# Kernel optimization log

Measured on AMD Instinct MI355X. Metric: run time of the kernel, lower is better.

The kernel has to match this reference:

```python
import jax, jax.numpy as jnp
import numpy as np

EPS = 1e-5
NUM_HEADS = 12
MAX_TEXT_LEN = 40

def ln(x, g, b):
    m = x.mean(-1, keepdims=True)
    v = ((x - m) ** 2).mean(-1, keepdims=True)
    return (x - m) / jnp.sqrt(v + EPS) * g + b

def mlp(x, w1, b1, w2, b2):
    h = jax.nn.gelu(x @ w1.T + b1, approximate=False)  # torch nn.GELU default = exact
    return h @ w2.T + b2

def setup_inputs() -> dict:
    key = jax.random.key(0)
    ks = jax.random.split(key, 16)
    B, N, C, H, HID = 16, 616, 768, 12, 3072
    s = 0.02
    d = {}
    d["x"] = jax.random.normal(ks[0], (B, N, C), jnp.float32)
    d["rel_bias"] = jax.random.normal(ks[1], (H, N, N), jnp.float32)
    d["ln1_g"] = jnp.ones(C, jnp.float32); d["ln1_b"] = jnp.zeros(C, jnp.float32)
    d["w_qkv"] = jax.random.normal(ks[2], (3 * C, C), jnp.float32) * s
    d["q_bias"] = jnp.zeros(C, jnp.float32); d["v_bias"] = jnp.zeros(C, jnp.float32)
    d["w_proj"] = jax.random.normal(ks[3], (C, C), jnp.float32) * s
    d["b_proj"] = jnp.zeros(C, jnp.float32)
    d["gamma1"] = 0.1 * jnp.ones(C, jnp.float32)
    d["gamma2"] = 0.1 * jnp.ones(C, jnp.float32)
    d["ln2t_g"] = jnp.ones(C, jnp.float32); d["ln2t_b"] = jnp.zeros(C, jnp.float32)
    d["ln2i_g"] = jnp.ones(C, jnp.float32); d["ln2i_b"] = jnp.zeros(C, jnp.float32)
    d["wt1"] = jax.random.normal(ks[4], (HID, C), jnp.float32) * s
    d["bt1"] = jnp.zeros(HID, jnp.float32)
    d["wt2"] = jax.random.normal(ks[5], (C, HID), jnp.float32) * s
    d["bt2"] = jnp.zeros(C, jnp.float32)
    d["wi1"] = jax.random.normal(ks[6], (HID, C), jnp.float32) * s
    d["bi1"] = jnp.zeros(HID, jnp.float32)
    d["wi2"] = jax.random.normal(ks[7], (C, HID), jnp.float32) * s
    d["bi2"] = jnp.zeros(C, jnp.float32)
    return d

def reference(x, rel_bias, ln1_g, ln1_b, w_qkv, q_bias, v_bias, w_proj, b_proj,
              gamma1, gamma2, ln2t_g, ln2t_b, ln2i_g, ln2i_b,
              wt1, bt1, wt2, bt2, wi1, bi1, wi2, bi2):
    B, N, C = x.shape
    H = NUM_HEADS
    hd = C // H
    scale = hd ** -0.5
    # --- attention ---
    n = ln(x, ln1_g, ln1_b)
    qkv_bias = jnp.concatenate([q_bias, jnp.zeros_like(v_bias), v_bias])
    qkv = (n @ w_qkv.T + qkv_bias).reshape(B, N, 3, H, hd).transpose(2, 0, 3, 1, 4)
    q, k, v = qkv[0] * scale, qkv[1], qkv[2]  # [B,H,N,hd]
    attn = jnp.einsum('bhqd,bhkd->bhqk', q.astype(jnp.float32), k.astype(jnp.float32))
    attn = attn + rel_bias  # rel_bias [H,N,N] broadcasts over B
    attn = jax.nn.softmax(attn, axis=-1).astype(x.dtype)
    o = jnp.einsum('bhqk,bhkd->bhqd', attn, v).transpose(0, 2, 1, 3).reshape(B, N, C)
    o = o @ w_proj.T + b_proj
    x = x + gamma1 * o
    # --- modality-split MLP (modality_type is None, no vl-ffn) ---
    xt = x[:, :MAX_TEXT_LEN]
    xi = x[:, MAX_TEXT_LEN:]
    xt = xt + gamma2 * mlp(ln(xt, ln2t_g, ln2t_b), wt1, bt1, wt2, bt2)
    xi = xi + gamma2 * mlp(ln(xi, ln2i_g, ln2i_b), wi1, bi1, wi2, bi2)
    return jnp.concatenate([xt, xi], axis=1)
```

## Files before the change

### kernel.cpp

```cpp
#include <hip/hip_runtime.h>
#include <hip/hip_bf16.h>
#include <stdint.h>
#include <math.h>

#define AS1 __attribute__((address_space(1)))
#define AS3 __attribute__((address_space(3)))

typedef __bf16 bf16_t;
typedef __bf16 bf16x8 __attribute__((ext_vector_type(8)));
typedef float f32x4 __attribute__((ext_vector_type(4)));

static constexpr int B_ = 16, N_ = 616, C_ = 768, H_ = 12, HD = 64, HID = 3072;
static constexpr int NP = 640;
static constexpr int M_REAL = B_ * N_;
static constexpr int M_PAD = 9984;
static constexpr int NT_ = 40, NI_ = 576;

__device__ __forceinline__ void gl_lds16(const void* g, void* l) {
  __builtin_amdgcn_global_load_lds((const AS1 void*)(uintptr_t)g,
                                   (AS3 void*)(uint32_t)(uintptr_t)l, 16, 0, 0);
}
__device__ __forceinline__ f32x4 mfma16(bf16x8 a, bf16x8 b, f32x4 c) {
  return __builtin_amdgcn_mfma_f32_16x16x32_bf16(a, b, c, 0, 0, 0);
}
__device__ __forceinline__ float gelu_f(float x) {
  float u = x * (0.7978845608f + 0.0356774081f * x * x);
  return x / (1.f + __expf(-2.f * u));
}

struct CastArgs {
  const float* src[7];
  bf16_t* dst[7];
  int n4[7];
};

__global__ __launch_bounds__(256) void cast_all(CastArgs a, int total4) {
  int i = blockIdx.x * blockDim.x + threadIdx.x;
  int st = gridDim.x * blockDim.x;
  for (; i < total4; i += st) {
    int off = i;
#pragma unroll
    for (int s = 0; s < 7; ++s) {
      if (off < a.n4[s]) {
        float4 v = ((const float4*)a.src[s])[off];
        float sub = (s == 6) ? 8.f : 0.f;
        bf16_t* d = a.dst[s] + (size_t)off * 4;
        d[0] = (bf16_t)(v.x - sub); d[1] = (bf16_t)(v.y - sub);
        d[2] = (bf16_t)(v.z - sub); d[3] = (bf16_t)(v.w - sub);
        break;
      }
      off -= a.n4[s];
    }
  }
}

__global__ __launch_bounds__(256) void ln_rows(const float* __restrict__ x,
                                               const float* __restrict__ g,
                                               const float* __restrict__ b,
                                               bf16_t* __restrict__ out) {
  int r = blockIdx.x, t = threadIdx.x;
  bf16_t* orow = out + (size_t)r * C_;
  const float* xr = x + (size_t)r * C_;
  float v0 = xr[t], v1 = xr[t + 256], v2 = xr[t + 512];
  float s = v0 + v1 + v2, ss = v0 * v0 + v1 * v1 + v2 * v2;
#pragma unroll
  for (int off = 32; off > 0; off >>= 1) { s += __shfl_xor(s, off); ss += __shfl_xor(ss, off); }
  __shared__ float sm[8];
  int w = t >> 6;
  if ((t & 63) == 0) { sm[w] = s; sm[4 + w] = ss; }
  __syncthreads();
  s = sm[0] + sm[1] + sm[2] + sm[3];
  ss = sm[4] + sm[5] + sm[6] + sm[7];
  float mean = s * (1.f / C_);
  float var = ss * (1.f / C_) - mean * mean;
  float ri = rsqrtf(var + 1e-5f);
  orow[t]       = (bf16_t)((v0 - mean) * ri * g[t]       + b[t]);
  orow[t + 256] = (bf16_t)((v1 - mean) * ri * g[t + 256] + b[t + 256]);
  orow[t + 512] = (bf16_t)((v2 - mean) * ri * g[t + 512] + b[t + 512]);
}

__global__ __launch_bounds__(256) void ln2_pack(const float* __restrict__ x1,
                                                const float* __restrict__ gt, const float* __restrict__ bt,
                                                const float* __restrict__ gi, const float* __restrict__ bi,
                                                bf16_t* __restrict__ out) {
  int m = blockIdx.x, t = threadIdx.x;
  if (m >= M_REAL) {
    bf16_t* orow = out + (size_t)(640 + (m - M_REAL)) * C_;
    orow[t] = (bf16_t)0.f; orow[t+256] = (bf16_t)0.f; orow[t+512] = (bf16_t)0.f;
    return;
  }
  int b_ = m / N_, nn = m - b_ * N_;
  const float* g; const float* bb; int dest;
  if (nn < NT_) { dest = b_ * NT_ + nn; g = gt; bb = bt; }
  else          { dest = 768 + b_ * NI_ + (nn - NT_); g = gi; bb = bi; }
  const float* xr = x1 + (size_t)m * C_;
  float v0 = xr[t], v1 = xr[t + 256], v2 = xr[t + 512];
  float s = v0 + v1 + v2, ss = v0 * v0 + v1 * v1 + v2 * v2;
#pragma unroll
  for (int off = 32; off > 0; off >>= 1) { s += __shfl_xor(s, off); ss += __shfl_xor(ss, off); }
  __shared__ float sm[8];
  int w = t >> 6;
  if ((t & 63) == 0) { sm[w] = s; sm[4 + w] = ss; }
  __syncthreads();
  s = sm[0] + sm[1] + sm[2] + sm[3];
  ss = sm[4] + sm[5] + sm[6] + sm[7];
  float mean = s * (1.f / C_);
  float var = ss * (1.f / C_) - mean * mean;
  float ri = rsqrtf(var + 1e-5f);
  bf16_t* orow = out + (size_t)dest * C_;
  orow[t]       = (bf16_t)((v0 - mean) * ri * g[t]       + bb[t]);
  orow[t + 256] = (bf16_t)((v1 - mean) * ri * g[t + 256] + bb[t + 256]);
  orow[t + 512] = (bf16_t)((v2 - mean) * ri * g[t + 512] + bb[t + 512]);
}

__global__ __launch_bounds__(256) void transpose_v(const bf16_t* __restrict__ v,
                                                   bf16_t* __restrict__ vT) {
  __shared__ bf16_t t[64][80];
  int n0 = blockIdx.x * 64, bh = blockIdx.y;
  int tid = threadIdx.x;
  int r0 = tid >> 2, c0 = (tid & 3) * 16;
  int n = n0 + r0;
#pragma unroll
  for (int cc = 0; cc < 2; ++cc) {
    bf16x8 vv;
    if (n < N_) vv = *(const bf16x8*)(v + ((size_t)bh * N_ + n) * HD + c0 + cc * 8);
    else {
#pragma unroll
      for (int e = 0; e < 8; ++e) vv[e] = (bf16_t)0.f;
    }
#pragma unroll
    for (int e = 0; e < 8; ++e) t[c0 + cc * 8 + e][r0] = vv[e];
  }
  __syncthreads();
  int d = tid >> 2, nc = (tid & 3) * 16;
  bf16_t* dst = vT + ((size_t)(bh * HD + d)) * NP + n0 + nc;
  *(bf16x8*)dst       = *(const bf16x8*)&t[d][nc];
  *(bf16x8*)(dst + 8) = *(const bf16x8*)&t[d][nc + 8];
}

struct EpiP {
  const float* bias;
  const float* bias_i;
  const float* bias2;
  const float* gamma;
  const float* xres;
  float* outf;
  bf16_t* ob0;
  bf16_t* ob1;
  bf16_t* ob2;
};

template <int EPI>
__global__ __launch_bounds__(256, 3) void gemm128(const bf16_t* __restrict__ A,
                                                  const bf16_t* __restrict__ Bt,
                                                  const bf16_t* __restrict__ Bi,
                                                  int K, int MBc, int nb, int tb, EpiP P) {
  __shared__ bf16_t As[8192], Bs[8192];
  const int tid = threadIdx.x, lane = tid & 63, w = tid >> 6;
  const int l16 = lane & 15, lq = lane >> 4;
  const int wr = w >> 1, wc = w & 1;
  const int NTk = K >> 6;

  int mblk, nblk;
  {
    int nwg = MBc * nb;
    int bid = blockIdx.x;
    int q8 = nwg >> 3, r8 = nwg & 7;
    int xcd = bid & 7, sidx = bid >> 3;
    int wg = (xcd < r8 ? xcd * (q8 + 1) : r8 * (q8 + 1) + (xcd - r8) * q8) + sidx;
    mblk = wg / nb; nblk = wg - mblk * nb;
  }
  const int m0 = mblk * 128, n0 = nblk * 128;
  const bf16_t* Bw = (mblk < tb) ? Bt : Bi;

  f32x4 acc[4][4] = {};

  const int swsrc = ((lane & 7) ^ ((lane >> 3) & 7)) * 8;
  size_t aoff[4], boff[4];
  int ldsoff[4];
#pragma unroll
  for (int j = 0; j < 4; ++j) {
    int srow = j * 32 + w * 8 + (lane >> 3);
    aoff[j] = (size_t)(m0 + srow) * K + swsrc;
    boff[j] = (size_t)(n0 + srow) * K + swsrc;
    ldsoff[j] = (j * 256 + w * 64) * 8;
  }
  const int sw0 = ((0 * 4 + lq) ^ (l16 & 7)) * 8;
  const int sw1 = ((1 * 4 + lq) ^ (l16 & 7)) * 8;
  const int rbA = (wr * 64 + l16) * 64;
  const int rbB = (wc * 64 + l16) * 64;

  for (int t = 0; t < NTk; ++t) {
    const size_t kadd = (size_t)t * 64;
#pragma unroll
    for (int j = 0; j < 4; ++j) gl_lds16(A + aoff[j] + kadd, As + ldsoff[j]);
#pragma unroll
    for (int j = 0; j < 4; ++j) gl_lds16(Bw + boff[j] + kadd, Bs + ldsoff[j]);
    __syncthreads();

    bf16x8 av[4][2], bv[4][2];
#pragma unroll
    for (int i = 0; i < 4; ++i) {
      av[i][0] = *(const bf16x8*)(As + rbA + i * 1024 + sw0);
      av[i][1] = *(const bf16x8*)(As + rbA + i * 1024 + sw1);
      bv[i][0] = *(const bf16x8*)(Bs + rbB + i * 1024 + sw0);
      bv[i][1] = *(const bf16x8*)(Bs + rbB + i * 1024 + sw1);
    }
#pragma unroll
    for (int kk = 0; kk < 2; ++kk)
#pragma unroll
      for (int i = 0; i < 4; ++i)
#pragma unroll
        for (int j = 0; j < 4; ++j)
          acc[i][j] = mfma16(av[i][kk], bv[j][kk], acc[i][j]);
    __syncthreads();
  }

  const float* bsel = (mblk < tb) ? P.bias : P.bias_i;
  (void)bsel;
  int which = n0 / C_;
#pragma unroll
  for (int i = 0; i < 4; ++i) {
    int mb = m0 + wr * 64 + i * 16 + lq * 4;
#pragma unroll
    for (int j = 0; j < 4; ++j) {
      int jc = n0 + wc * 64 + j * 16 + l16;
#pragma unroll
      for (int rr = 0; rr < 4; ++rr) {
        int m = mb + rr;
        float v = acc[i][j][rr];
        if constexpr (EPI == 0) {
          int b_ = m / N_, nn = m - b_ * N_;
          int jj = jc - which * C_;
          int hh = jj >> 6, d = jj & 63;
          int bh = b_ * H_ + hh;
          if (which == 0) {
            P.ob0[((size_t)bh * NP + nn) * HD + d] = (bf16_t)((v + P.bias[jj]) * 0.125f);
          } else if (which == 1) {
            P.ob1[((size_t)bh * NP + nn) * HD + d] = (bf16_t)v;
          } else {
            P.ob2[((size_t)bh * N_ + nn) * HD + d] = (bf16_t)(v + P.bias2[jj]);
          }
        } else if constexpr (EPI == 1) {
          size_t idx = (size_t)m * C_ + jc;
          P.outf[idx] = P.xres[idx] + P.gamma[jc] * (v + P.bias[jc]);
        } else if constexpr (EPI == 2) {
          P.ob0[(size_t)m * HID + jc] = (bf16_t)gelu_f(v + bsel[jc]);
        } else {
          int orig = -1;
          if (m < 640)      orig = (m / NT_) * N_ + (m - (m / NT_) * NT_);
          else if (m >= 768) {
            int mi = m - 768;
            int bb = mi / NI_;
            orig = bb * N_ + NT_ + (mi - bb * NI_);
          }
          if (orig >= 0) {
            size_t idx = (size_t)orig * C_ + jc;
            P.outf[idx] = P.xres[idx] + P.gamma[jc] * (v + bsel[jc]);
          }
        }
      }
    }
  }
}

__global__ __launch_bounds__(256) void attn_fwd(const bf16_t* __restrict__ qb,
                                                const bf16_t* __restrict__ kb,
                                                const bf16_t* __restrict__ vT,
                                                const bf16_t* __restrict__ biasb,
                                                bf16_t* __restrict__ o_mat) {
  __shared__ bf16_t qs[64 * 64];
  __shared__ bf16_t ks[2][64 * 64], vs[2][64 * 64];
  __shared__ bf16_t ps[4][16 * 72];
  const int tid = threadIdx.x, lane = tid & 63, w = tid >> 6;
  const int l16 = lane & 15, lq = lane >> 4;
  int wg = (blockIdx.x & 7) * 240 + (blockIdx.x >> 3);
  const int qt = wg % 10;
  const int rb = wg / 10;
  const int b_ = rb & 15, h = rb >> 4;
  const int bh = b_ * H_ + h;
  const int q0 = qt * 64;
  const int swr = (l16 & 7);
  constexpr int NKT = NP / 64;

  const bf16_t* ksrc = kb + (size_t)bh * NP * HD;
  const bf16_t* vsrc = vT + (size_t)bh * HD * NP;

  auto stage_kv = [&](int c, int kt) {
    int n0k = kt * 64;
#pragma unroll
    for (int it = 0; it < 2; ++it) {
      int cb = it * 256 + w * 64, cc = cb + lane;
      int row = cc >> 3, sg = (cc & 7) ^ ((cc >> 3) & 7);
      gl_lds16(ksrc + ((size_t)(n0k + row)) * HD + sg * 8, ks[c] + cb * 8);
      gl_lds16(vsrc + (size_t)row * NP + n0k + sg * 8, vs[c] + cb * 8);
    }
  };

  const bf16_t* qsrc = qb + ((size_t)bh * NP + q0) * HD;
#pragma unroll
  for (int it = 0; it < 2; ++it) {
    int cb = it * 256 + w * 64, c = cb + lane;
    int row = c >> 3, sg = (c & 7) ^ ((c >> 3) & 7);
    gl_lds16(qsrc + row * 64 + sg * 8, qs + cb * 8);
  }
  stage_kv(0, 0);
  __syncthreads();

  bf16x8 aq[2];
  aq[0] = *(const bf16x8*)(qs + (w * 16 + l16) * 64 + ((0 * 4 + lq) ^ swr) * 8);
  aq[1] = *(const bf16x8*)(qs + (w * 16 + l16) * 64 + ((1 * 4 + lq) ^ swr) * 8);

  float lsum[4] = {0.f, 0.f, 0.f, 0.f};
  f32x4 oacc[4] = {};
  const int qrow_base = q0 + w * 16 + lq * 4;

  const bf16_t* bp[4];
#pragma unroll
  for (int r = 0; r < 4; ++r) {
    int qg = qrow_base + r;
    int qc = qg < N_ ? qg : (N_ - 1);
    bp[r] = biasb + (size_t)h * N_ * N_ + (size_t)qc * N_;
  }

  for (int kt = 0; kt < NKT; ++kt) {
    const int c = kt & 1;
    if (kt > 0) __syncthreads();
    if (kt + 1 < NKT) stage_kv(c ^ 1, kt + 1);

    f32x4 sf[4];
#pragma unroll
    for (int f = 0; f < 4; ++f) {
      f32x4 z = {};
#pragma unroll
      for (int kk = 0; kk < 2; ++kk) {
        bf16x8 bk = *(const bf16x8*)(ks[c] + (f * 16 + l16) * 64 + ((kk * 4 + lq) ^ swr) * 8);
        z = mfma16(aq[kk], bk, z);
      }
      sf[f] = z;
    }

    int n0k = kt * 64;
    bf16_t* psw = ps[w];
    if (kt < NKT - 1) {
#pragma unroll
      for (int f = 0; f < 4; ++f) {
        int kc = n0k + f * 16 + l16;
#pragma unroll
        for (int r = 0; r < 4; ++r) {
          float p = __expf(sf[f][r] + (float)bp[r][kc]);
          lsum[r] += p;
          psw[(lq * 4 + r) * 72 + f * 16 + l16] = (bf16_t)p;
        }
      }
    } else {
#pragma unroll
      for (int f = 0; f < 4; ++f) {
        int kc = n0k + f * 16 + l16;
        bool ok = kc < N_;
        int kcs = ok ? kc : 0;
#pragma unroll
        for (int r = 0; r < 4; ++r) {
          float p = ok ? __expf(sf[f][r] + (float)bp[r][kcs]) : 0.f;
          lsum[r] += p;
          psw[(lq * 4 + r) * 72 + f * 16 + l16] = (bf16_t)p;
        }
      }
    }

#pragma unroll
    for (int kk = 0; kk < 2; ++kk) {
      bf16x8 pa = *(const bf16x8*)(psw + l16 * 72 + kk * 32 + lq * 8);
#pragma unroll
      for (int df = 0; df < 4; ++df) {
        bf16x8 bv = *(const bf16x8*)(vs[c] + (df * 16 + l16) * 64 + ((kk * 4 + lq) ^ swr) * 8);
        oacc[df] = mfma16(pa, bv, oacc[df]);
      }
    }
  }

#pragma unroll
  for (int off = 1; off < 16; off <<= 1)
#pragma unroll
    for (int r = 0; r < 4; ++r)
      lsum[r] += __shfl_xor(lsum[r], off, 16);

#pragma unroll
  for (int r = 0; r < 4; ++r) {
    int qg = qrow_base + r;
    if (qg < N_) {
      float rl = 1.f / lsum[r];
      size_t orow = ((size_t)(b_ * N_ + qg)) * C_ + h * HD;
#pragma unroll
      for (int df = 0; df < 4; ++df)
        o_mat[orow + df * 16 + l16] = (bf16_t)(oacc[df][r] * rl);
    }
  }
}

extern "C" void kernel_launch(void* const* d_in, const int* in_sizes, int n_in,
                              void* d_out, int out_size, void* d_ws, size_t ws_size,
                              hipStream_t stream) {
  const float* x      = (const float*)d_in[0];
  const float* rel    = (const float*)d_in[1];
  const float* ln1_g  = (const float*)d_in[2];
  const float* ln1_b  = (const float*)d_in[3];
  const float* w_qkv  = (const float*)d_in[4];
  const float* q_bias = (const float*)d_in[5];
  const float* v_bias = (const float*)d_in[6];
  const float* w_proj = (const float*)d_in[7];
  const float* b_proj = (const float*)d_in[8];
  const float* gamma1 = (const float*)d_in[9];
  const float* gamma2 = (const float*)d_in[10];
  const float* ln2t_g = (const float*)d_in[11];
  const float* ln2t_b = (const float*)d_in[12];
  const float* ln2i_g = (const float*)d_in[13];
  const float* ln2i_b = (const float*)d_in[14];
  const float* wt1    = (const float*)d_in[15];
  const float* bt1    = (const float*)d_in[16];
  const float* wt2    = (const float*)d_in[17];
  const float* bt2    = (const float*)d_in[18];
  const float* wi1    = (const float*)d_in[19];
  const float* bi1    = (const float*)d_in[20];
  const float* wi2    = (const float*)d_in[21];
  const float* bi2    = (const float*)d_in[22];
  float* out = (float*)d_out;

  char* ws = (char*)d_ws;
  bf16_t* wqkvb  = (bf16_t*)(ws + 0);
  bf16_t* wprojb = (bf16_t*)(ws + 3538944);
  bf16_t* wt1b   = (bf16_t*)(ws + 4718592);
  bf16_t* wi1b   = (bf16_t*)(ws + 9437184);
  bf16_t* wt2b   = (bf16_t*)(ws + 14155776);
  bf16_t* wi2b   = (bf16_t*)(ws + 18874368);
  bf16_t* n1     = (bf16_t*)(ws + 23592960);
  float*  x1     = (float*) (ws + 38928384);
  bf16_t* qbuf   = (bf16_t*)(ws + 69206016);
  bf16_t* kbuf   = (bf16_t*)(ws + 84934656);
  bf16_t* vTbuf  = (bf16_t*)(ws + 100663296);
  bf16_t* biasb  = (bf16_t*)(ws + 116391936);
  bf16_t* vtmp   = (bf16_t*)(ws + 38928384);
  bf16_t* o_mat  = n1;
  bf16_t* n2p    = n1;
  bf16_t* hbuf   = qbuf;

  {
    CastArgs a;
    a.src[0] = w_qkv;  a.dst[0] = wqkvb;  a.n4[0] = (3 * C_ * C_) / 4;
    a.src[1] = w_proj; a.dst[1] = wprojb; a.n4[1] = (C_ * C_) / 4;
    a.src[2] = wt1;    a.dst[2] = wt1b;   a.n4[2] = (HID * C_) / 4;
    a.src[3] = wi1;    a.dst[3] = wi1b;   a.n4[3] = (HID * C_) / 4;
    a.src[4] = wt2;    a.dst[4] = wt2b;   a.n4[4] = (C_ * HID) / 4;
    a.src[5] = wi2;    a.dst[5] = wi2b;   a.n4[5] = (C_ * HID) / 4;
    a.src[6] = rel;    a.dst[6] = biasb;  a.n4[6] = (H_ * N_ * N_) / 4;
    int total4 = a.n4[0] + a.n4[1] + a.n4[2] + a.n4[3] + a.n4[4] + a.n4[5] + a.n4[6];
    cast_all<<<2048, 256, 0, stream>>>(a, total4);
  }
  ln_rows<<<M_REAL, 256, 0, stream>>>(x, ln1_g, ln1_b, n1);

  {
    EpiP P{}; P.bias = q_bias; P.bias2 = v_bias;
    P.ob0 = qbuf; P.ob1 = kbuf; P.ob2 = vtmp;
    gemm128<0><<<77 * 18, 256, 0, stream>>>(n1, wqkvb, wqkvb, C_, 77, 18, 0, P);
  }
  transpose_v<<<dim3(NP / 64, B_ * H_), 256, 0, stream>>>(vtmp, vTbuf);
  attn_fwd<<<1920, 256, 0, stream>>>(qbuf, kbuf, vTbuf, biasb, o_mat);

  {
    EpiP P{}; P.bias = b_proj; P.bias_i = b_proj; P.gamma = gamma1; P.xres = x; P.outf = x1;
    gemm128<1><<<77 * 6, 256, 0, stream>>>(o_mat, wprojb, wprojb, C_, 77, 6, 0, P);
  }
  ln2_pack<<<M_PAD, 256, 0, stream>>>(x1, ln2t_g, ln2t_b, ln2i_g, ln2i_b, n2p);

  {
    EpiP P{}; P.bias = bt1; P.bias_i = bi1; P.ob0 = hbuf;
    gemm128<2><<<78 * 24, 256, 0, stream>>>(n2p, wt1b, wi1b, C_, 78, 24, 6, P);
  }
  {
    EpiP P{}; P.bias = bt2; P.bias_i = bi2; P.gamma = gamma2; P.xres = x1; P.outf = out;
    gemm128<3><<<78 * 6, 256, 0, stream>>>(hbuf, wt2b, wi2b, HID, 78, 6, 6, P);
  }
}
```

Before: 316.9 us.

## Shrink GEMM M-tile to 64 rows with 1x4 warp layout for more workgroups

Replaces the 128x128 GEMM tile with a 64x128 tile. Each of the four waves now owns all 64 rows and a 32-column slice, so the warp layout changes from 2x2 to 1x4, LDS staging and epilogue indexing are redone, and launch bounds are raised to allow four blocks per CU. All four GEMM launches double their M-block count, and the text/image split index moves to match. The aim is more workgroups and better occupancy and CU fill on the small-N GEMMs, at the cost of lower arithmetic intensity and more B-tile reloads from memory.

Result: no change. 312.4 us (-1.4%).

```diff
diff --git a/kernel.cpp b/kernel.cpp
--- a/kernel.cpp
+++ b/kernel.cpp
@@ -151,14 +151,13 @@
 };
 
 template <int EPI>
-__global__ __launch_bounds__(256, 3) void gemm128(const bf16_t* __restrict__ A,
-                                                  const bf16_t* __restrict__ Bt,
-                                                  const bf16_t* __restrict__ Bi,
-                                                  int K, int MBc, int nb, int tb, EpiP P) {
-  __shared__ bf16_t As[8192], Bs[8192];
+__global__ __launch_bounds__(256, 4) void gemm64(const bf16_t* __restrict__ A,
+                                                 const bf16_t* __restrict__ Bt,
+                                                 const bf16_t* __restrict__ Bi,
+                                                 int K, int MBc, int nb, int tb, EpiP P) {
+  __shared__ bf16_t As[4096], Bs[8192];
   const int tid = threadIdx.x, lane = tid & 63, w = tid >> 6;
   const int l16 = lane & 15, lq = lane >> 4;
-  const int wr = w >> 1, wc = w & 1;
   const int NTk = K >> 6;
 
   int mblk, nblk;
@@ -170,48 +169,56 @@
     int wg = (xcd < r8 ? xcd * (q8 + 1) : r8 * (q8 + 1) + (xcd - r8) * q8) + sidx;
     mblk = wg / nb; nblk = wg - mblk * nb;
   }
-  const int m0 = mblk * 128, n0 = nblk * 128;
+  const int m0 = mblk * 64, n0 = nblk * 128;
   const bf16_t* Bw = (mblk < tb) ? Bt : Bi;
 
-  f32x4 acc[4][4] = {};
+  f32x4 acc[4][2] = {};
 
   const int swsrc = ((lane & 7) ^ ((lane >> 3) & 7)) * 8;
-  size_t aoff[4], boff[4];
-  int ldsoff[4];
+  size_t aoff[2]; int aldso[2];
+  size_t boff[4]; int bldso[4];
+#pragma unroll
+  for (int j = 0; j < 2; ++j) {
+    int srow = w * 16 + j * 8 + (lane >> 3);
+    aoff[j] = (size_t)(m0 + srow) * K + swsrc;
+    aldso[j] = (w * 128 + j * 64) * 8;
+  }
 #pragma unroll
   for (int j = 0; j < 4; ++j) {
-    int srow = j * 32 + w * 8 + (lane >> 3);
-    aoff[j] = (size_t)(m0 + srow) * K + swsrc;
+    int srow = w * 32 + j * 8 + (lane >> 3);
     boff[j] = (size_t)(n0 + srow) * K + swsrc;
-    ldsoff[j] = (j * 256 + w * 64) * 8;
+    bldso[j] = (w * 256 + j * 64) * 8;
   }
   const int sw0 = ((0 * 4 + lq) ^ (l16 & 7)) * 8;
   const int sw1 = ((1 * 4 + lq) ^ (l16 & 7)) * 8;
-  const int rbA = (wr * 64 + l16) * 64;
-  const int rbB = (wc * 64 + l16) * 64;
+  const int rbA = l16 * 64;
+  const int rbB = (w * 32 + l16) * 64;
 
   for (int t = 0; t < NTk; ++t) {
     const size_t kadd = (size_t)t * 64;
 #pragma unroll
-    for (int j = 0; j < 4; ++j) gl_lds16(A + aoff[j] + kadd, As + ldsoff[j]);
-#pragma unroll
-    for (int j = 0; j < 4; ++j) gl_lds16(Bw + boff[j] + kadd, Bs + ldsoff[j]);
+    for (int j = 0; j < 2; ++j) gl_lds16(A + aoff[j] + kadd, As + aldso[j]);
+#pragma unroll
+    for (int j = 0; j < 4; ++j) gl_lds16(Bw + boff[j] + kadd, Bs + bldso[j]);
     __syncthreads();
 
-    bf16x8 av[4][2], bv[4][2];
+    bf16x8 av[4][2], bv[2][2];
 #pragma unroll
     for (int i = 0; i < 4; ++i) {
       av[i][0] = *(const bf16x8*)(As + rbA + i * 1024 + sw0);
       av[i][1] = *(const bf16x8*)(As + rbA + i * 1024 + sw1);
-      bv[i][0] = *(const bf16x8*)(Bs + rbB + i * 1024 + sw0);
-      bv[i][1] = *(const bf16x8*)(Bs + rbB + i * 1024 + sw1);
+    }
+#pragma unroll
+    for (int j = 0; j < 2; ++j) {
+      bv[j][0] = *(const bf16x8*)(Bs + rbB + j * 1024 + sw0);
+      bv[j][1] = *(const bf16x8*)(Bs + rbB + j * 1024 + sw1);
     }
 #pragma unroll
     for (int kk = 0; kk < 2; ++kk)
 #pragma unroll
       for (int i = 0; i < 4; ++i)
 #pragma unroll
-        for (int j = 0; j < 4; ++j)
+        for (int j = 0; j < 2; ++j)
           acc[i][j] = mfma16(av[i][kk], bv[j][kk], acc[i][j]);
     __syncthreads();
   }
@@ -221,10 +228,10 @@
   int which = n0 / C_;
 #pragma unroll
   for (int i = 0; i < 4; ++i) {
-    int mb = m0 + wr * 64 + i * 16 + lq * 4;
-#pragma unroll
-    for (int j = 0; j < 4; ++j) {
-      int jc = n0 + wc * 64 + j * 16 + l16;
+    int mb = m0 + i * 16 + lq * 4;
+#pragma unroll
+    for (int j = 0; j < 2; ++j) {
+      int jc = n0 + w * 32 + j * 16 + l16;
 #pragma unroll
       for (int rr = 0; rr < 4; ++rr) {
         int m = mb + rr;
@@ -461,23 +468,23 @@
   {
     EpiP P{}; P.bias = q_bias; P.bias2 = v_bias;
     P.ob0 = qbuf; P.ob1 = kbuf; P.ob2 = vtmp;
-    gemm128<0><<<77 * 18, 256, 0, stream>>>(n1, wqkvb, wqkvb, C_, 77, 18, 0, P);
+    gemm64<0><<<154 * 18, 256, 0, stream>>>(n1, wqkvb, wqkvb, C_, 154, 18, 0, P);
   }
   transpose_v<<<dim3(NP / 64, B_ * H_), 256, 0, stream>>>(vtmp, vTbuf);
   attn_fwd<<<1920, 256, 0, stream>>>(qbuf, kbuf, vTbuf, biasb, o_mat);
 
   {
     EpiP P{}; P.bias = b_proj; P.bias_i = b_proj; P.gamma = gamma1; P.xres = x; P.outf = x1;
-    gemm128<1><<<77 * 6, 256, 0, stream>>>(o_mat, wprojb, wprojb, C_, 77, 6, 0, P);
+    gemm64<1><<<154 * 6, 256, 0, stream>>>(o_mat, wprojb, wprojb, C_, 154, 6, 0, P);
   }
   ln2_pack<<<M_PAD, 256, 0, stream>>>(x1, ln2t_g, ln2t_b, ln2i_g, ln2i_b, n2p);
 
   {
     EpiP P{}; P.bias = bt1; P.bias_i = bi1; P.ob0 = hbuf;
-    gemm128<2><<<78 * 24, 256, 0, stream>>>(n2p, wt1b, wi1b, C_, 78, 24, 6, P);
+    gemm64<2><<<156 * 24, 256, 0, stream>>>(n2p, wt1b, wi1b, C_, 156, 24, 12, P);
   }
   {
     EpiP P{}; P.bias = bt2; P.bias_i = bi2; P.gamma = gamma2; P.xres = x1; P.outf = out;
-    gemm128<3><<<78 * 6, 256, 0, stream>>>(hbuf, wt2b, wi2b, HID, 78, 6, 6, P);
-  }
-}
+    gemm64<3><<<156 * 6, 256, 0, stream>>>(hbuf, wt2b, wi2b, HID, 156, 6, 12, P);
+  }
+}
```
